# Kernel tuning notes

Measured on AMD Instinct MI355X. Metric: run time of the kernel, lower is better.

The kernel has to match this reference:

```python
import jax, jax.numpy as jnp
import numpy as np

IN_CH, OUT_CH, SEQ_LEN, MODES = 512, 512, 4096, 64
B, L, H, E = 16, SEQ_LEN, 8, IN_CH // 8


def setup_inputs() -> dict:
    key = jax.random.key(0)
    kq, kk, kv, kwr, kwi = jax.random.split(key, 5)
    scale = 1.0 / (IN_CH * OUT_CH)
    return {
        "q": jax.random.normal(kq, (B, L, H, E), jnp.float32),
        "k": jax.random.normal(kk, (B, L, H, E), jnp.float32),
        "v": jax.random.normal(kv, (B, L, H, E), jnp.float32),
        "mask": jnp.ones((B, L), dtype=bool),
        # torch.rand(..., dtype=cfloat) fills real & imag parts uniform [0,1)
        "w_real": scale * jax.random.uniform(kwr, (8, IN_CH // 8, OUT_CH // 8, MODES), jnp.float32),
        "w_imag": scale * jax.random.uniform(kwi, (8, IN_CH // 8, OUT_CH // 8, MODES), jnp.float32),
    }


def reference(q, k, v, mask, w_real, w_imag):
    # k, v, mask are unused by SpectralConv1d.forward (signature parity only).
    Bq, Lq, Hq, Eq = q.shape
    M = w_real.shape[-1]          # number of retained frequency modes
    Eo = w_real.shape[2]          # out_channels // 8
    x = jnp.transpose(q, (0, 2, 3, 1))          # [B, H, E, L]
    x_ft = jnp.fft.rfft(x, axis=-1)             # [B, H, E, L//2+1] complex
    W = jax.lax.complex(w_real, w_imag)         # [H, E, Eo, M]
    # For modes1 < 1000 the index list is range(M), so the per-mode Python loop
    # is equivalent to one batched complex einsum over the first M modes.
    out_m = jnp.einsum('bhem,heom->bhom', x_ft[..., :M], W)  # [B, H, Eo, M]
    out_ft = jnp.zeros((Bq, Hq, Eo, Lq // 2 + 1), dtype=out_m.dtype)
    out_ft = out_ft.at[..., :M].set(out_m)
    x_out = jnp.fft.irfft(out_ft, n=Lq, axis=-1)  # [B, H, Eo, L] real
    return x_out  # original returns (x_out, None); second element is constant None
```

## Files before the change

kernel.cpp:

```cpp
#include <hip/hip_runtime.h>
#include <math.h>

#define TW1_OFF 0
#define TW2_OFF 262144
#define YH_OFF  524288
#define XP_OFF  1048576

typedef short s16x8 __attribute__((ext_vector_type(8)));
typedef float f32x4 __attribute__((ext_vector_type(4)));

__device__ inline unsigned short f2bf(float x) {
    union { float f; unsigned int u; } v; v.f = x;
    return (unsigned short)((v.u + 0x7fffu + ((v.u >> 16) & 1u)) >> 16);
}

__global__ __launch_bounds__(256) void k_tw(float* __restrict__ ws) {
    const int i = blockIdx.x * 256 + threadIdx.x;
    const float C = 1.53398078788564123e-3f;
    {
        const int j = i & 7, lane = (i >> 3) & 63, mt = (i >> 9) & 7, tch = i >> 12;
        const int fh = mt * 16 + (lane & 15);
        const int t  = tch * 32 + ((lane >> 4) << 3) + j;
        const int f  = fh & 63;
        float s, c;
        sincosf((float)((f * t) & 4095) * C, &s, &c);
        ((unsigned short*)(ws + TW1_OFF))[i] = f2bf(fh < 64 ? c : -s);
    }
    {
        const int j = i & 7, lane = (i >> 3) & 63, ks = (i >> 9) & 3, nt = (i >> 11) & 7, tc = i >> 14;
        const int t  = tc * 128 + nt * 16 + (lane & 15);
        const int fh = ks * 32 + ((lane >> 4) << 3) + j;
        const int f  = fh >> 1;
        float s, c;
        sincosf((float)((f * t) & 4095) * C, &s, &c);
        const float sc = (f ? 2.0f : 1.0f) * (1.0f / 4096.0f);
        ((unsigned short*)(ws + TW2_OFF))[i] = f2bf((fh & 1) ? -sc * s : sc * c);
    }
}

__global__ __launch_bounds__(256) void k_dft(const float* __restrict__ q,
                                             float* __restrict__ ws) {
    const int bid = blockIdx.x;
    const int kc = bid >> 7, bh = bid & 127;
    const int b = bh >> 3, h = bh & 7;
    const int tid = threadIdx.x;
    const int lane = tid & 63, w = tid >> 6;
    const int wm = w >> 1, wn = w & 1;
    const int l15 = lane & 15, qd = lane >> 4;

    const s16x8* __restrict__ tw1 = (const s16x8*)(ws + TW1_OFF);
    const float* __restrict__ qb = q + (size_t)b * 2097152 + h * 64;

    f32x4 acc[4][2];
#pragma unroll
    for (int mt = 0; mt < 4; ++mt)
#pragma unroll
        for (int nt = 0; nt < 2; ++nt)
            acc[mt][nt] = (f32x4){0.f, 0.f, 0.f, 0.f};

    for (int it = 0; it < 16; ++it) {
        const int tch0 = kc * 32 + it * 2;
        s16x8 afr[4][2];
#pragma unroll
        for (int mt = 0; mt < 4; ++mt)
#pragma unroll
            for (int ks = 0; ks < 2; ++ks)
                afr[mt][ks] = tw1[(size_t)((tch0 + ks) * 8 + wm * 4 + mt) * 64 + lane];

        const int tbase = kc * 1024 + it * 64;
        s16x8 bfr[2][2];
#pragma unroll
        for (int nt = 0; nt < 2; ++nt) {
            const int e = wn * 32 + nt * 16 + l15;
#pragma unroll
            for (int ks = 0; ks < 2; ++ks) {
                const float* qp = qb + (size_t)(tbase + ks * 32 + qd * 8) * 512 + e;
#pragma unroll
                for (int j = 0; j < 8; ++j)
                    bfr[nt][ks][j] = (short)f2bf(qp[(size_t)j * 512]);
            }
        }
#pragma unroll
        for (int ks = 0; ks < 2; ++ks)
#pragma unroll
            for (int mt = 0; mt < 4; ++mt)
#pragma unroll
                for (int nt = 0; nt < 2; ++nt)
                    acc[mt][nt] = __builtin_amdgcn_mfma_f32_16x16x32_bf16(
                        afr[mt][ks], bfr[nt][ks], acc[mt][nt], 0, 0, 0);
    }
    float* xp = ws + XP_OFF + (size_t)(kc * 128 + bh) * 8192;
#pragma unroll
    for (int mt = 0; mt < 4; ++mt)
#pragma unroll
        for (int nt = 0; nt < 2; ++nt) {
            const int e = wn * 32 + nt * 16 + l15;
#pragma unroll
            for (int r = 0; r < 4; ++r) {
                const int fh = (wm * 4 + mt) * 16 + qd * 4 + r;
                xp[fh * 64 + e] = acc[mt][nt][r];
            }
        }
}

__global__ __launch_bounds__(256) void k_mix(const float* __restrict__ wr_g,
                                             const float* __restrict__ wi_g,
                                             float* __restrict__ ws) {
    __shared__ float lds_x[64][69];
    const int bid = blockIdx.x;
    const int bh = bid >> 1, f0 = (bid & 1) * 32;
    const int h = bh & 7;
    const int tid = threadIdx.x;
    const float* xp = ws + XP_OFF;
#pragma unroll
    for (int p = 0; p < 2; ++p)
#pragma unroll
        for (int k2 = 0; k2 < 8; ++k2) {
            const int idx = tid + k2 * 256;
            const int fl = idx >> 6, e = idx & 63;
            const int row = p * 64 + f0 + fl;
            float s = 0.f;
#pragma unroll
            for (int kc = 0; kc < 4; ++kc)
                s += xp[(size_t)(kc * 128 + bh) * 8192 + row * 64 + e];
            lds_x[e][fl + p * 34] = s;
        }
    __syncthreads();
    const int fl = tid & 31, og = tid >> 5;
    const int f = f0 + fl;
    float yr[8], yi[8];
#pragma unroll
    for (int oo = 0; oo < 8; ++oo) { yr[oo] = 0.f; yi[oo] = 0.f; }
    const float* wrp = wr_g + (size_t)h * 262144 + og * 64 + f;
    const float* wip = wi_g + (size_t)h * 262144 + og * 64 + f;
    for (int e = 0; e < 64; ++e) {
        const float xr = lds_x[e][fl], xi = lds_x[e][fl + 34];
        const float* wre = wrp + (size_t)e * 4096;
        const float* wie = wip + (size_t)e * 4096;
#pragma unroll
        for (int oo = 0; oo < 8; ++oo) {
            const float wr = wre[oo * 512];
            const float wi = wie[oo * 512];
            yr[oo] += xr * wr - xi * wi;
            yi[oo] += xr * wi + xi * wr;
        }
    }
    unsigned short* yh = (unsigned short*)(ws + YH_OFF);
#pragma unroll
    for (int oo = 0; oo < 8; ++oo) {
        const int o = og + 8 * oo;
        const int mt = o >> 4, ol = o & 15;
#pragma unroll
        for (int ri = 0; ri < 2; ++ri) {
            const int fh = 2 * f + ri;
            const float v = ri ? yi[oo] : yr[oo];
            yh[((size_t)((bh * 4 + mt) * 4 + (fh >> 5)) * 64 + ((fh >> 3) & 3) * 16 + ol) * 8 + (fh & 7)] = f2bf(v);
        }
    }
}

__global__ __launch_bounds__(256) void k_inv(float* __restrict__ out,
                                             const float* __restrict__ ws) {
    const int bid = blockIdx.x;
    const int tc = bid >> 7, bh = bid & 127;
    const int tid = threadIdx.x, lane = tid & 63, w = tid >> 6;
    const int l15 = lane & 15, qd = lane >> 4;
    const s16x8* __restrict__ ya = (const s16x8*)(ws + YH_OFF);
    const s16x8* __restrict__ tb = (const s16x8*)(ws + TW2_OFF);
    f32x4 acc[4][2];
#pragma unroll
    for (int mt = 0; mt < 4; ++mt)
#pragma unroll
        for (int nt = 0; nt < 2; ++nt)
            acc[mt][nt] = (f32x4){0.f, 0.f, 0.f, 0.f};
#pragma unroll
    for (int ks = 0; ks < 4; ++ks) {
        s16x8 af[4], bfv[2];
#pragma unroll
        for (int mt = 0; mt < 4; ++mt)
            af[mt] = ya[(size_t)((bh * 4 + mt) * 4 + ks) * 64 + lane];
#pragma unroll
        for (int nt = 0; nt < 2; ++nt)
            bfv[nt] = tb[(size_t)((tc * 8 + w * 2 + nt) * 4 + ks) * 64 + lane];
#pragma unroll
        for (int mt = 0; mt < 4; ++mt)
#pragma unroll
            for (int nt = 0; nt < 2; ++nt)
                acc[mt][nt] = __builtin_amdgcn_mfma_f32_16x16x32_bf16(
                    af[mt], bfv[nt], acc[mt][nt], 0, 0, 0);
    }
    float* ob = out + (size_t)bh * 262144 + tc * 128 + w * 32;
#pragma unroll
    for (int mt = 0; mt < 4; ++mt)
#pragma unroll
        for (int nt = 0; nt < 2; ++nt)
#pragma unroll
            for (int r = 0; r < 4; ++r) {
                const int o = mt * 16 + qd * 4 + r;
                ob[(size_t)o * 4096 + nt * 16 + l15] = acc[mt][nt][r];
            }
}

extern "C" void kernel_launch(void* const* d_in, const int* in_sizes, int n_in,
                              void* d_out, int out_size, void* d_ws, size_t ws_size,
                              hipStream_t stream) {
    const float* q  = (const float*)d_in[0];
    const float* wr = (const float*)d_in[4];
    const float* wi = (const float*)d_in[5];
    float* out = (float*)d_out;
    float* ws  = (float*)d_ws;

    k_tw <<<2048, 256, 0, stream>>>(ws);
    k_dft<<<512,  256, 0, stream>>>(q, ws);
    k_mix<<<256,  256, 0, stream>>>(wr, wi, ws);
    k_inv<<<4096, 256, 0, stream>>>(out, ws);
}
```

Measured before the change: 450.5 us.

## Swap inverse MFMA operands for vector nontemporal stores; widen mix kernel

The inverse DFT kernel swaps MFMA operand roles so each lane's accumulator holds four consecutive time samples. Output is then written with 16-byte nontemporal vector stores instead of scattered scalar stores. The mixing kernel doubles its block size to 512 threads, halving per-thread output channels. The forward DFT also reads q with nontemporal loads to reduce cache pollution from the streamed input.

```diff
diff --git a/kernel.cpp b/kernel.cpp
--- a/kernel.cpp
+++ b/kernel.cpp
@@ -77,7 +77,7 @@
                 const float* qp = qb + (size_t)(tbase + ks * 32 + qd * 8) * 512 + e;
 #pragma unroll
                 for (int j = 0; j < 8; ++j)
-                    bfr[nt][ks][j] = (short)f2bf(qp[(size_t)j * 512]);
+                    bfr[nt][ks][j] = (short)f2bf(__builtin_nontemporal_load(qp + (size_t)j * 512));
             }
         }
 #pragma unroll
@@ -103,7 +103,7 @@
         }
 }
 
-__global__ __launch_bounds__(256) void k_mix(const float* __restrict__ wr_g,
+__global__ __launch_bounds__(512) void k_mix(const float* __restrict__ wr_g,
                                              const float* __restrict__ wi_g,
                                              float* __restrict__ ws) {
     __shared__ float lds_x[64][69];
@@ -113,24 +113,23 @@
     const int tid = threadIdx.x;
     const float* xp = ws + XP_OFF;
 #pragma unroll
-    for (int p = 0; p < 2; ++p)
-#pragma unroll
-        for (int k2 = 0; k2 < 8; ++k2) {
-            const int idx = tid + k2 * 256;
-            const int fl = idx >> 6, e = idx & 63;
-            const int row = p * 64 + f0 + fl;
-            float s = 0.f;
-#pragma unroll
-            for (int kc = 0; kc < 4; ++kc)
-                s += xp[(size_t)(kc * 128 + bh) * 8192 + row * 64 + e];
-            lds_x[e][fl + p * 34] = s;
-        }
+    for (int k2 = 0; k2 < 8; ++k2) {
+        const int idx = tid + k2 * 512;
+        const int flp = idx >> 6, e = idx & 63;
+        const int p = flp >> 5, fl = flp & 31;
+        const int row = p * 64 + f0 + fl;
+        float s = 0.f;
+#pragma unroll
+        for (int kc = 0; kc < 4; ++kc)
+            s += xp[(size_t)(kc * 128 + bh) * 8192 + row * 64 + e];
+        lds_x[e][fl + p * 34] = s;
+    }
     __syncthreads();
     const int fl = tid & 31, og = tid >> 5;
     const int f = f0 + fl;
-    float yr[8], yi[8];
-#pragma unroll
-    for (int oo = 0; oo < 8; ++oo) { yr[oo] = 0.f; yi[oo] = 0.f; }
+    float yr[4], yi[4];
+#pragma unroll
+    for (int oo = 0; oo < 4; ++oo) { yr[oo] = 0.f; yi[oo] = 0.f; }
     const float* wrp = wr_g + (size_t)h * 262144 + og * 64 + f;
     const float* wip = wi_g + (size_t)h * 262144 + og * 64 + f;
     for (int e = 0; e < 64; ++e) {
@@ -138,17 +137,17 @@
         const float* wre = wrp + (size_t)e * 4096;
         const float* wie = wip + (size_t)e * 4096;
 #pragma unroll
-        for (int oo = 0; oo < 8; ++oo) {
-            const float wr = wre[oo * 512];
-            const float wi = wie[oo * 512];
+        for (int oo = 0; oo < 4; ++oo) {
+            const float wr = wre[oo * 1024];
+            const float wi = wie[oo * 1024];
             yr[oo] += xr * wr - xi * wi;
             yi[oo] += xr * wi + xi * wr;
         }
     }
     unsigned short* yh = (unsigned short*)(ws + YH_OFF);
 #pragma unroll
-    for (int oo = 0; oo < 8; ++oo) {
-        const int o = og + 8 * oo;
+    for (int oo = 0; oo < 4; ++oo) {
+        const int o = og + 16 * oo;
         const int mt = o >> 4, ol = o & 15;
 #pragma unroll
         for (int ri = 0; ri < 2; ++ri) {
@@ -167,38 +166,37 @@
     const int l15 = lane & 15, qd = lane >> 4;
     const s16x8* __restrict__ ya = (const s16x8*)(ws + YH_OFF);
     const s16x8* __restrict__ tb = (const s16x8*)(ws + TW2_OFF);
-    f32x4 acc[4][2];
-#pragma unroll
-    for (int mt = 0; mt < 4; ++mt)
-#pragma unroll
-        for (int nt = 0; nt < 2; ++nt)
-            acc[mt][nt] = (f32x4){0.f, 0.f, 0.f, 0.f};
+    f32x4 acc[2][4];
+#pragma unroll
+    for (int tt = 0; tt < 2; ++tt)
+#pragma unroll
+        for (int ot = 0; ot < 4; ++ot)
+            acc[tt][ot] = (f32x4){0.f, 0.f, 0.f, 0.f};
 #pragma unroll
     for (int ks = 0; ks < 4; ++ks) {
-        s16x8 af[4], bfv[2];
-#pragma unroll
-        for (int mt = 0; mt < 4; ++mt)
-            af[mt] = ya[(size_t)((bh * 4 + mt) * 4 + ks) * 64 + lane];
-#pragma unroll
-        for (int nt = 0; nt < 2; ++nt)
-            bfv[nt] = tb[(size_t)((tc * 8 + w * 2 + nt) * 4 + ks) * 64 + lane];
-#pragma unroll
-        for (int mt = 0; mt < 4; ++mt)
-#pragma unroll
-            for (int nt = 0; nt < 2; ++nt)
-                acc[mt][nt] = __builtin_amdgcn_mfma_f32_16x16x32_bf16(
-                    af[mt], bfv[nt], acc[mt][nt], 0, 0, 0);
+        s16x8 af[2], bfv[4];
+#pragma unroll
+        for (int tt = 0; tt < 2; ++tt)
+            af[tt] = tb[(size_t)((tc * 8 + w * 2 + tt) * 4 + ks) * 64 + lane];
+#pragma unroll
+        for (int ot = 0; ot < 4; ++ot)
+            bfv[ot] = ya[(size_t)((bh * 4 + ot) * 4 + ks) * 64 + lane];
+#pragma unroll
+        for (int tt = 0; tt < 2; ++tt)
+#pragma unroll
+            for (int ot = 0; ot < 4; ++ot)
+                acc[tt][ot] = __builtin_amdgcn_mfma_f32_16x16x32_bf16(
+                    af[tt], bfv[ot], acc[tt][ot], 0, 0, 0);
     }
     float* ob = out + (size_t)bh * 262144 + tc * 128 + w * 32;
 #pragma unroll
-    for (int mt = 0; mt < 4; ++mt)
-#pragma unroll
-        for (int nt = 0; nt < 2; ++nt)
-#pragma unroll
-            for (int r = 0; r < 4; ++r) {
-                const int o = mt * 16 + qd * 4 + r;
-                ob[(size_t)o * 4096 + nt * 16 + l15] = acc[mt][nt][r];
-            }
+    for (int tt = 0; tt < 2; ++tt)
+#pragma unroll
+        for (int ot = 0; ot < 4; ++ot) {
+            const int o = ot * 16 + l15;
+            float* p = ob + (size_t)o * 4096 + tt * 16 + qd * 4;
+            __builtin_nontemporal_store(acc[tt][ot], (f32x4*)p);
+        }
 }
 
 extern "C" void kernel_launch(void* const* d_in, const int* in_sizes, int n_in,
@@ -212,6 +210,6 @@
 
     k_tw <<<2048, 256, 0, stream>>>(ws);
     k_dft<<<512,  256, 0, stream>>>(q, ws);
-    k_mix<<<256,  256, 0, stream>>>(wr, wi, ws);
+    k_mix<<<256,  512, 0, stream>>>(wr, wi, ws);
     k_inv<<<4096, 256, 0, stream>>>(out, ws);
 }
```

New measurement: 450.1 us. About the same (-0.1%).
